# Performance work log

Hardware: AMD Instinct MI355X
Metric: run time of the kernel (lower is better)

Reference implementation:

```python
import jax, jax.numpy as jnp
import numpy as np

N_SAMPLES = 200            # points sampled per ray (n_points in source)
T_HASH = 1 << 19           # hash table size per level (log2_hashmap_size=19)
_PRIMES = jnp.array([1, 2654435761, 805459861], dtype=jnp.uint32)
_CORNERS = jnp.array([[i, j, k] for i in (0, 1) for j in (0, 1) for k in (0, 1)], dtype=jnp.int32)  # [8,3]


def sample_points_along_ray(start, end):
    # start/end: [B,2] in [0,1]. Lerp xy along the ray, z = normalized depth t.
    t = jnp.linspace(0.0, 1.0, N_SAMPLES, dtype=start.dtype)           # [S]
    xy = start[:, None, :] * (1.0 - t)[None, :, None] + end[:, None, :] * t[None, :, None]  # [B,S,2]
    z = jnp.broadcast_to(t[None, :, None], (start.shape[0], N_SAMPLES, 1))
    return jnp.concatenate([xy, z], axis=-1)                            # [B,S,3]


def grid_encode(pts, tables, base_res):
    # pts: [N,3] in [0,1]; tables: [L, T_HASH, D]. Multi-res hash grid + trilinear interp.
    L = tables.shape[0]
    outs = []
    for l in range(L):
        res = base_res * (2 ** l)
        xf = pts * res
        x0 = jnp.floor(xf).astype(jnp.int32)
        w = xf - x0                                                     # [N,3] trilinear weights
        c = x0[:, None, :] + _CORNERS[None]                             # [N,8,3]
        h = c.astype(jnp.uint32) * _PRIMES[None, None, :]
        idx = (h[..., 0] ^ h[..., 1] ^ h[..., 2]) & jnp.uint32(T_HASH - 1)  # [N,8]
        cw = jnp.prod(jnp.where(_CORNERS[None].astype(bool), w[:, None, :], 1.0 - w[:, None, :]), axis=-1)  # [N,8]
        feat = tables[l][idx.astype(jnp.int32)]                         # [N,8,D] gather
        outs.append(jnp.sum(feat * cw[..., None], axis=1))              # [N,D]
    return jnp.concatenate(outs, axis=-1)


def setup_inputs() -> dict:
    key = jax.random.key(0)
    ks = jax.random.split(key, 13)
    B = 16384
    return {
        "x": jax.random.uniform(ks[0], (B, 4), dtype=jnp.float32),
        "table_label": jax.random.normal(ks[1], (5, T_HASH, 1), dtype=jnp.float32),
        "table_rgb": jax.random.normal(ks[2], (6, T_HASH, 4), dtype=jnp.float32),
        "w_label": jax.random.normal(ks[3], (5, 1), dtype=jnp.float32),
        "b_label": jax.random.normal(ks[4], (1,), dtype=jnp.float32),
        "W1": jax.random.normal(ks[5], (120, 64), dtype=jnp.float32) * 0.1,
        "b1": jax.random.normal(ks[6], (64,), dtype=jnp.float32) * 0.1,
        "W2": jax.random.normal(ks[7], (64, 64), dtype=jnp.float32) * 0.1,
        "b2": jax.random.normal(ks[8], (64,), dtype=jnp.float32) * 0.1,
        "W3": jax.random.normal(ks[9], (64, 64), dtype=jnp.float32) * 0.1,
        "b3": jax.random.normal(ks[10], (64,), dtype=jnp.float32) * 0.1,
        "W4": jax.random.normal(ks[11], (64, 3), dtype=jnp.float32) * 0.1,
        "b4": jax.random.normal(ks[12], (3,), dtype=jnp.float32) * 0.1,
    }


def reference(x, table_label, table_rgb, w_label, b_label, W1, b1, W2, b2, W3, b3, W4, b4):
    B = x.shape[0]
    pts = sample_points_along_ray(x[:, :2], x[:, 2:4]).reshape(-1, 3)   # [B*S,3]
    enc_l = grid_encode(pts, table_label, 8).reshape(B, N_SAMPLES, -1)  # [B,S,5]
    label = jax.nn.sigmoid(enc_l @ w_label + b_label)                   # [B,S,1]
    hits = jnp.max(label, axis=1)                                       # [B,1]
    first = jnp.argmax((label > 0.5).astype(jnp.float32), axis=1).reshape(-1)  # [B]
    enc_r = grid_encode(pts, table_rgb, 4).reshape(B, N_SAMPLES, -1)    # [B,S,24]
    rows = jnp.arange(B)
    maxi = N_SAMPLES - 1

    def gather(off):
        return enc_r[rows, jnp.clip(first + off, 0, maxi)]              # [B,24]

    feat = jnp.concatenate([gather(-2), gather(-1), gather(0), gather(1), gather(2)], axis=-1)  # [B,120]
    h = jax.nn.relu(feat @ W1 + b1)
    h = jax.nn.relu(h @ W2 + b2)
    h = jax.nn.relu(h @ W3 + b3)
    rgb = h @ W4 + b4                                                   # [B,3]
    return hits, label, rgb
```

## Files before the change

### kernel.cpp

```cpp
#include <hip/hip_runtime.h>
#include <math.h>
#include <stdint.h>

#define NS 200
#define THASH (1 << 19)
#define TMASK ((1u << 19) - 1u)

__device__ __forceinline__ float sigmoidf_(float v) {
    return 1.0f / (1.0f + __expf(-v));
}

__global__ __launch_bounds__(256) void k_label(
        const float* __restrict__ x,
        const float* __restrict__ tlab,
        const float* __restrict__ wlab, const float* __restrict__ blab,
        float* __restrict__ hits, float* __restrict__ labels,
        int* __restrict__ firsts)
{
    const uint32_t P2 = 2654435761u, P3 = 805459861u;
    const int b = blockIdx.x;
    const int tid = threadIdx.x;
    const int lane = tid & 63;
    const int wid = tid >> 6;
    const float4 ray = *(const float4*)(x + 4 * (size_t)b);

    const int s_eff = tid < NS ? tid : NS - 1;
    const float t = (float)s_eff * (1.0f / 199.0f);
    const float px = ray.x * (1.0f - t) + ray.z * t;
    const float py = ray.y * (1.0f - t) + ray.w * t;
    const float pz = t;

    float acc = blab[0];
    #pragma unroll
    for (int l = 0; l < 5; ++l) {
        const float res = (float)(8 << l);
        const float xf = px * res, yf = py * res, zf = pz * res;
        const float fx = floorf(xf), fy = floorf(yf), fz = floorf(zf);
        const float wx = xf - fx, wy = yf - fy, wz = zf - fz;
        const uint32_t x0 = (uint32_t)(int)fx;
        const uint32_t y0 = (uint32_t)(int)fy;
        const uint32_t z0 = (uint32_t)(int)fz;

        const uint32_t cell = x0 | (y0 << 10) | (z0 << 20);
        const uint32_t prevc = __shfl_up(cell, 1);
        const bool leader = (lane == 0) || (prevc != cell);
        const uint64_t bal = __ballot(leader);
        const uint64_t below = bal & (~0ull >> (63 - lane));
        const int ldr = 63 - __clzll(below);

        float v0 = 0.f, v1 = 0.f, v2 = 0.f, v3 = 0.f,
              v4 = 0.f, v5 = 0.f, v6 = 0.f, v7 = 0.f;
        if (leader) {
            const uint32_t hx0 = x0,      hx1 = x0 + 1u;
            const uint32_t hy0 = y0 * P2, hy1 = hy0 + P2;
            const uint32_t hz0 = z0 * P3, hz1 = hz0 + P3;
            const float* __restrict__ tl = tlab + (size_t)l * THASH;
            v0 = tl[(hx0 ^ hy0 ^ hz0) & TMASK];
            v1 = tl[(hx0 ^ hy0 ^ hz1) & TMASK];
            v2 = tl[(hx0 ^ hy1 ^ hz0) & TMASK];
            v3 = tl[(hx0 ^ hy1 ^ hz1) & TMASK];
            v4 = tl[(hx1 ^ hy0 ^ hz0) & TMASK];
            v5 = tl[(hx1 ^ hy0 ^ hz1) & TMASK];
            v6 = tl[(hx1 ^ hy1 ^ hz0) & TMASK];
            v7 = tl[(hx1 ^ hy1 ^ hz1) & TMASK];
        }
        v0 = __shfl(v0, ldr); v1 = __shfl(v1, ldr);
        v2 = __shfl(v2, ldr); v3 = __shfl(v3, ldr);
        v4 = __shfl(v4, ldr); v5 = __shfl(v5, ldr);
        v6 = __shfl(v6, ldr); v7 = __shfl(v7, ldr);

        const float c00 = fmaf(wz, v1 - v0, v0);
        const float c01 = fmaf(wz, v3 - v2, v2);
        const float c10 = fmaf(wz, v5 - v4, v4);
        const float c11 = fmaf(wz, v7 - v6, v6);
        const float c0 = fmaf(wy, c01 - c00, c00);
        const float c1 = fmaf(wy, c11 - c10, c10);
        const float cv = fmaf(wx, c1 - c0, c0);
        acc = fmaf(cv, wlab[l], acc);
    }

    float lab = -1.0f;
    int cand = NS;
    if (tid < NS) {
        lab = sigmoidf_(acc);
        labels[(size_t)b * NS + tid] = lab;
        if (lab > 0.5f) cand = tid;
    }

    __shared__ float wmax[4];
    __shared__ int wmin[4];
    float m = lab;
    int c = cand;
    #pragma unroll
    for (int off = 32; off > 0; off >>= 1) {
        m = fmaxf(m, __shfl_xor(m, off));
        c = min(c, __shfl_xor(c, off));
    }
    if (lane == 0) { wmax[wid] = m; wmin[wid] = c; }
    __syncthreads();
    if (tid == 0) {
        float mm = fmaxf(fmaxf(wmax[0], wmax[1]), fmaxf(wmax[2], wmax[3]));
        int cc = min(min(wmin[0], wmin[1]), min(wmin[2], wmin[3]));
        hits[b] = mm;
        firsts[b] = (cc >= NS) ? 0 : cc;
    }
}

__global__ __launch_bounds__(256) void k_rgb(
        const float* __restrict__ x,
        const float* __restrict__ trgb,
        const int* __restrict__ firsts,
        const float* __restrict__ W1, const float* __restrict__ b1,
        const float* __restrict__ W2, const float* __restrict__ b2,
        const float* __restrict__ W3, const float* __restrict__ b3,
        const float* __restrict__ W4, const float* __restrict__ b4,
        float* __restrict__ rgb)
{
    const uint32_t P2 = 2654435761u, P3 = 805459861u;
    const int wid = threadIdx.x >> 6;
    const int lane = threadIdx.x & 63;
    const int b = blockIdx.x * 4 + wid;

    __shared__ float feat[4][120];
    __shared__ float hs[4][64];

    const float4 ray = *(const float4*)(x + 4 * (size_t)b);
    const int first = firsts[b];

    const int corner = lane & 7;
    const int group = lane >> 3;
    const int bi = (corner >> 2) & 1, bj = (corner >> 1) & 1, bk = corner & 1;

    #pragma unroll
    for (int it = 0; it < 4; ++it) {
        const int pair = it * 8 + group;
        float vx = 0.f, vy = 0.f, vz = 0.f, vw = 0.f;
        if (pair < 30) {
            const int si = pair / 6;
            const int l = pair % 6;
            int sc = first + si - 2;
            sc = sc < 0 ? 0 : (sc > NS - 1 ? NS - 1 : sc);
            const float t = (float)sc * (1.0f / 199.0f);
            const float px = ray.x * (1.0f - t) + ray.z * t;
            const float py = ray.y * (1.0f - t) + ray.w * t;
            const float pz = t;
            const int res = 4 << l;
            const float xf = px * (float)res, yf = py * (float)res, zf = pz * (float)res;
            const float fx = floorf(xf), fy = floorf(yf), fz = floorf(zf);
            const float wx = xf - fx, wy = yf - fy, wz = zf - fz;
            const uint32_t x0 = (uint32_t)(int)fx, y0 = (uint32_t)(int)fy, z0 = (uint32_t)(int)fz;
            const uint32_t hx = x0 + (uint32_t)bi;
            const uint32_t hy = (y0 + (uint32_t)bj) * P2;
            const uint32_t hz = (z0 + (uint32_t)bk) * P3;
            const uint32_t idx = (hx ^ hy ^ hz) & TMASK;
            const float cw = (bi ? wx : 1.0f - wx) * (bj ? wy : 1.0f - wy) * (bk ? wz : 1.0f - wz);
            const float4 tv = *(const float4*)(trgb + (((size_t)l << 19) + idx) * 4);
            vx = tv.x * cw; vy = tv.y * cw; vz = tv.z * cw; vw = tv.w * cw;
        }
        #pragma unroll
        for (int m = 1; m < 8; m <<= 1) {
            vx += __shfl_xor(vx, m);
            vy += __shfl_xor(vy, m);
            vz += __shfl_xor(vz, m);
            vw += __shfl_xor(vw, m);
        }
        if (corner == 0 && pair < 30) {
            const int si = pair / 6, l = pair % 6;
            float* f = &feat[wid][si * 24 + l * 4];
            f[0] = vx; f[1] = vy; f[2] = vz; f[3] = vw;
        }
    }
    __syncthreads();

    const float* fw = feat[wid];
    float a0 = b1[lane], a1 = 0.f, a2 = 0.f, a3 = 0.f;
    #pragma unroll
    for (int i = 0; i < 120; i += 4) {
        const float4 fv = *(const float4*)(fw + i);
        a0 = fmaf(fv.x, W1[(i + 0) * 64 + lane], a0);
        a1 = fmaf(fv.y, W1[(i + 1) * 64 + lane], a1);
        a2 = fmaf(fv.z, W1[(i + 2) * 64 + lane], a2);
        a3 = fmaf(fv.w, W1[(i + 3) * 64 + lane], a3);
    }
    float h = fmaxf((a0 + a1) + (a2 + a3), 0.0f);

    hs[wid][lane] = h;
    __syncthreads();
    a0 = b2[lane]; a1 = 0.f; a2 = 0.f; a3 = 0.f;
    #pragma unroll
    for (int i = 0; i < 64; i += 4) {
        const float4 hv = *(const float4*)(&hs[wid][i]);
        a0 = fmaf(hv.x, W2[(i + 0) * 64 + lane], a0);
        a1 = fmaf(hv.y, W2[(i + 1) * 64 + lane], a1);
        a2 = fmaf(hv.z, W2[(i + 2) * 64 + lane], a2);
        a3 = fmaf(hv.w, W2[(i + 3) * 64 + lane], a3);
    }
    h = fmaxf((a0 + a1) + (a2 + a3), 0.0f);

    __syncthreads();
    hs[wid][lane] = h;
    __syncthreads();
    a0 = b3[lane]; a1 = 0.f; a2 = 0.f; a3 = 0.f;
    #pragma unroll
    for (int i = 0; i < 64; i += 4) {
        const float4 hv = *(const float4*)(&hs[wid][i]);
        a0 = fmaf(hv.x, W3[(i + 0) * 64 + lane], a0);
        a1 = fmaf(hv.y, W3[(i + 1) * 64 + lane], a1);
        a2 = fmaf(hv.z, W3[(i + 2) * 64 + lane], a2);
        a3 = fmaf(hv.w, W3[(i + 3) * 64 + lane], a3);
    }
    h = fmaxf((a0 + a1) + (a2 + a3), 0.0f);

    __syncthreads();
    hs[wid][lane] = h;
    __syncthreads();
    if (lane < 3) {
        float r = b4[lane];
        #pragma unroll 8
        for (int j = 0; j < 64; ++j) r = fmaf(hs[wid][j], W4[j * 3 + lane], r);
        rgb[(size_t)b * 3 + lane] = r;
    }
}

extern "C" void kernel_launch(void* const* d_in, const int* in_sizes, int n_in,
                              void* d_out, int out_size, void* d_ws, size_t ws_size,
                              hipStream_t stream) {
    const float* x    = (const float*)d_in[0];
    const float* tlab = (const float*)d_in[1];
    const float* trgb = (const float*)d_in[2];
    const float* wlab = (const float*)d_in[3];
    const float* blab = (const float*)d_in[4];
    const float* W1   = (const float*)d_in[5];
    const float* b1   = (const float*)d_in[6];
    const float* W2   = (const float*)d_in[7];
    const float* b2   = (const float*)d_in[8];
    const float* W3   = (const float*)d_in[9];
    const float* b3   = (const float*)d_in[10];
    const float* W4   = (const float*)d_in[11];
    const float* b4   = (const float*)d_in[12];

    const int B = in_sizes[0] / 4;

    float* hits   = (float*)d_out;
    float* labels = hits + B;
    float* rgbout = labels + (size_t)B * NS;
    int* firsts   = (int*)d_ws;

    k_label<<<B, 256, 0, stream>>>(x, tlab, wlab, blab, hits, labels, firsts);
    k_rgb<<<B / 4, 256, 0, stream>>>(x, trgb, firsts,
                                     W1, b1, W2, b2, W3, b3, W4, b4, rgbout);
}
```

Baseline: 120.5 us.

## Derive coarse-level cells from finest grid and batch MLP over 16 rays per block

In the label kernel, the finest-level cell coordinates are computed once and the coarser levels' cells are obtained by right-shifting them. Leader detection uses a masked XOR of neighbouring cells, and the hash corners are built from XOR deltas. The finest level skips the ballot/shuffle dedup and loads directly. In the RGB kernel each block now handles 16 rays, with each wave computing 4 rays per MLP layer so that every weight load is reused across 4 rays. The intent is to cut per-level ALU work and weight traffic, at the cost of more shared memory and registers per block.

```diff
diff --git a/kernel.cpp b/kernel.cpp
--- a/kernel.cpp
+++ b/kernel.cpp
@@ -30,53 +30,90 @@
     const float py = ray.y * (1.0f - t) + ray.w * t;
     const float pz = t;
 
+    const float xf4 = px * 128.0f, yf4 = py * 128.0f, zf4 = pz * 128.0f;
+    const float fx4 = floorf(xf4), fy4 = floorf(yf4), fz4 = floorf(zf4);
+    const uint32_t x4 = (uint32_t)(int)fx4;
+    const uint32_t y4 = (uint32_t)(int)fy4;
+    const uint32_t z4 = (uint32_t)(int)fz4;
+    const uint32_t cell4 = x4 | (y4 << 10) | (z4 << 20);
+    const uint32_t prev = __shfl_up(cell4, 1);
+    const uint32_t diff = cell4 ^ prev;
+
     float acc = blab[0];
+
     #pragma unroll
-    for (int l = 0; l < 5; ++l) {
-        const float res = (float)(8 << l);
-        const float xf = px * res, yf = py * res, zf = pz * res;
-        const float fx = floorf(xf), fy = floorf(yf), fz = floorf(zf);
-        const float wx = xf - fx, wy = yf - fy, wz = zf - fz;
-        const uint32_t x0 = (uint32_t)(int)fx;
-        const uint32_t y0 = (uint32_t)(int)fy;
-        const uint32_t z0 = (uint32_t)(int)fz;
-
-        const uint32_t cell = x0 | (y0 << 10) | (z0 << 20);
-        const uint32_t prevc = __shfl_up(cell, 1);
-        const bool leader = (lane == 0) || (prevc != cell);
+    for (int l = 0; l < 4; ++l) {
+        const int k = 4 - l;
+        const uint32_t fm = 0x3FFu & ~((1u << k) - 1u);
+        const uint32_t m_l = fm | (fm << 10) | (fm << 20);
+        const bool leader = (lane == 0) || ((diff & m_l) != 0u);
         const uint64_t bal = __ballot(leader);
         const uint64_t below = bal & (~0ull >> (63 - lane));
         const int ldr = 63 - __clzll(below);
 
+        const uint32_t x0 = x4 >> k, y0 = y4 >> k, z0 = z4 >> k;
+        const float sc = 1.0f / (float)(1 << k);
+        const float wx = fmaf(xf4, sc, -(float)x0);
+        const float wy = fmaf(yf4, sc, -(float)y0);
+        const float wz = fmaf(zf4, sc, -(float)z0);
+
         float v0 = 0.f, v1 = 0.f, v2 = 0.f, v3 = 0.f,
-              v4 = 0.f, v5 = 0.f, v6 = 0.f, v7 = 0.f;
+              v4v = 0.f, v5 = 0.f, v6 = 0.f, v7 = 0.f;
         if (leader) {
-            const uint32_t hx0 = x0,      hx1 = x0 + 1u;
-            const uint32_t hy0 = y0 * P2, hy1 = hy0 + P2;
-            const uint32_t hz0 = z0 * P3, hz1 = hz0 + P3;
+            const uint32_t hy0 = y0 * P2, hz0 = z0 * P3;
+            const uint32_t base = x0 ^ hy0 ^ hz0;
+            const uint32_t dx = x0 ^ (x0 + 1u);
+            const uint32_t dy = hy0 ^ (hy0 + P2);
+            const uint32_t dz = hz0 ^ (hz0 + P3);
             const float* __restrict__ tl = tlab + (size_t)l * THASH;
-            v0 = tl[(hx0 ^ hy0 ^ hz0) & TMASK];
-            v1 = tl[(hx0 ^ hy0 ^ hz1) & TMASK];
-            v2 = tl[(hx0 ^ hy1 ^ hz0) & TMASK];
-            v3 = tl[(hx0 ^ hy1 ^ hz1) & TMASK];
-            v4 = tl[(hx1 ^ hy0 ^ hz0) & TMASK];
-            v5 = tl[(hx1 ^ hy0 ^ hz1) & TMASK];
-            v6 = tl[(hx1 ^ hy1 ^ hz0) & TMASK];
-            v7 = tl[(hx1 ^ hy1 ^ hz1) & TMASK];
-        }
-        v0 = __shfl(v0, ldr); v1 = __shfl(v1, ldr);
-        v2 = __shfl(v2, ldr); v3 = __shfl(v3, ldr);
-        v4 = __shfl(v4, ldr); v5 = __shfl(v5, ldr);
-        v6 = __shfl(v6, ldr); v7 = __shfl(v7, ldr);
+            v0  = tl[ base                 & TMASK];
+            v1  = tl[(base ^ dz)           & TMASK];
+            v2  = tl[(base ^ dy)           & TMASK];
+            v3  = tl[(base ^ dy ^ dz)      & TMASK];
+            v4v = tl[(base ^ dx)           & TMASK];
+            v5  = tl[(base ^ dx ^ dz)      & TMASK];
+            v6  = tl[(base ^ dx ^ dy)      & TMASK];
+            v7  = tl[(base ^ dx ^ dy ^ dz) & TMASK];
+        }
+        v0  = __shfl(v0, ldr);  v1 = __shfl(v1, ldr);
+        v2  = __shfl(v2, ldr);  v3 = __shfl(v3, ldr);
+        v4v = __shfl(v4v, ldr); v5 = __shfl(v5, ldr);
+        v6  = __shfl(v6, ldr);  v7 = __shfl(v7, ldr);
 
         const float c00 = fmaf(wz, v1 - v0, v0);
         const float c01 = fmaf(wz, v3 - v2, v2);
-        const float c10 = fmaf(wz, v5 - v4, v4);
+        const float c10 = fmaf(wz, v5 - v4v, v4v);
         const float c11 = fmaf(wz, v7 - v6, v6);
         const float c0 = fmaf(wy, c01 - c00, c00);
         const float c1 = fmaf(wy, c11 - c10, c10);
         const float cv = fmaf(wx, c1 - c0, c0);
         acc = fmaf(cv, wlab[l], acc);
+    }
+
+    {
+        const float wx = xf4 - fx4, wy = yf4 - fy4, wz = zf4 - fz4;
+        const uint32_t hy0 = y4 * P2, hz0 = z4 * P3;
+        const uint32_t base = x4 ^ hy0 ^ hz0;
+        const uint32_t dx = x4 ^ (x4 + 1u);
+        const uint32_t dy = hy0 ^ (hy0 + P2);
+        const uint32_t dz = hz0 ^ (hz0 + P3);
+        const float* __restrict__ tl = tlab + (size_t)4 * THASH;
+        const float v0  = tl[ base                 & TMASK];
+        const float v1  = tl[(base ^ dz)           & TMASK];
+        const float v2  = tl[(base ^ dy)           & TMASK];
+        const float v3  = tl[(base ^ dy ^ dz)      & TMASK];
+        const float v4v = tl[(base ^ dx)           & TMASK];
+        const float v5  = tl[(base ^ dx ^ dz)      & TMASK];
+        const float v6  = tl[(base ^ dx ^ dy)      & TMASK];
+        const float v7  = tl[(base ^ dx ^ dy ^ dz) & TMASK];
+        const float c00 = fmaf(wz, v1 - v0, v0);
+        const float c01 = fmaf(wz, v3 - v2, v2);
+        const float c10 = fmaf(wz, v5 - v4v, v4v);
+        const float c11 = fmaf(wz, v7 - v6, v6);
+        const float c0 = fmaf(wy, c01 - c00, c00);
+        const float c1 = fmaf(wy, c11 - c10, c10);
+        const float cv = fmaf(wx, c1 - c0, c0);
+        acc = fmaf(cv, wlab[4], acc);
     }
 
     float lab = -1.0f;
@@ -106,6 +143,7 @@
     }
 }
 
+#define RPB 16
 __global__ __launch_bounds__(256) void k_rgb(
         const float* __restrict__ x,
         const float* __restrict__ trgb,
@@ -117,108 +155,137 @@
         float* __restrict__ rgb)
 {
     const uint32_t P2 = 2654435761u, P3 = 805459861u;
-    const int wid = threadIdx.x >> 6;
-    const int lane = threadIdx.x & 63;
-    const int b = blockIdx.x * 4 + wid;
-
-    __shared__ float feat[4][120];
-    __shared__ float hs[4][64];
-
-    const float4 ray = *(const float4*)(x + 4 * (size_t)b);
-    const int first = firsts[b];
-
-    const int corner = lane & 7;
-    const int group = lane >> 3;
+    const int tid = threadIdx.x;
+    const int lane = tid & 63;
+    const int wid = tid >> 6;
+    const int rayBase = blockIdx.x * RPB;
+
+    __shared__ float feat[RPB][120];
+    __shared__ float hs[RPB][64];
+
+    const int corner = tid & 7;
+    const int rp = tid >> 3;
+    const int ray = rp >> 1;
+    const int pairHalf = rp & 1;
     const int bi = (corner >> 2) & 1, bj = (corner >> 1) & 1, bk = corner & 1;
 
+    const float4 rd = *(const float4*)(x + 4 * (size_t)(rayBase + ray));
+    const int first = firsts[rayBase + ray];
+
     #pragma unroll
-    for (int it = 0; it < 4; ++it) {
-        const int pair = it * 8 + group;
-        float vx = 0.f, vy = 0.f, vz = 0.f, vw = 0.f;
-        if (pair < 30) {
-            const int si = pair / 6;
-            const int l = pair % 6;
-            int sc = first + si - 2;
-            sc = sc < 0 ? 0 : (sc > NS - 1 ? NS - 1 : sc);
-            const float t = (float)sc * (1.0f / 199.0f);
-            const float px = ray.x * (1.0f - t) + ray.z * t;
-            const float py = ray.y * (1.0f - t) + ray.w * t;
-            const float pz = t;
-            const int res = 4 << l;
-            const float xf = px * (float)res, yf = py * (float)res, zf = pz * (float)res;
-            const float fx = floorf(xf), fy = floorf(yf), fz = floorf(zf);
-            const float wx = xf - fx, wy = yf - fy, wz = zf - fz;
-            const uint32_t x0 = (uint32_t)(int)fx, y0 = (uint32_t)(int)fy, z0 = (uint32_t)(int)fz;
-            const uint32_t hx = x0 + (uint32_t)bi;
-            const uint32_t hy = (y0 + (uint32_t)bj) * P2;
-            const uint32_t hz = (z0 + (uint32_t)bk) * P3;
-            const uint32_t idx = (hx ^ hy ^ hz) & TMASK;
-            const float cw = (bi ? wx : 1.0f - wx) * (bj ? wy : 1.0f - wy) * (bk ? wz : 1.0f - wz);
-            const float4 tv = *(const float4*)(trgb + (((size_t)l << 19) + idx) * 4);
-            vx = tv.x * cw; vy = tv.y * cw; vz = tv.z * cw; vw = tv.w * cw;
-        }
+    for (int it = 0; it < 15; ++it) {
+        const int pair = pairHalf * 15 + it;
+        const int si = pair / 6;
+        const int l = pair % 6;
+        int scl = first + si - 2;
+        scl = scl < 0 ? 0 : (scl > NS - 1 ? NS - 1 : scl);
+        const float t = (float)scl * (1.0f / 199.0f);
+        const float px = rd.x * (1.0f - t) + rd.z * t;
+        const float py = rd.y * (1.0f - t) + rd.w * t;
+        const float pz = t;
+        const int res = 4 << l;
+        const float xf = px * (float)res, yf = py * (float)res, zf = pz * (float)res;
+        const float fx = floorf(xf), fy = floorf(yf), fz = floorf(zf);
+        const float wx = xf - fx, wy = yf - fy, wz = zf - fz;
+        const uint32_t x0 = (uint32_t)(int)fx, y0 = (uint32_t)(int)fy, z0 = (uint32_t)(int)fz;
+        const uint32_t hx = x0 + (uint32_t)bi;
+        const uint32_t hy = (y0 + (uint32_t)bj) * P2;
+        const uint32_t hz = (z0 + (uint32_t)bk) * P3;
+        const uint32_t idx = (hx ^ hy ^ hz) & TMASK;
+        const float cw = (bi ? wx : 1.0f - wx) * (bj ? wy : 1.0f - wy) * (bk ? wz : 1.0f - wz);
+        const float4 tv = *(const float4*)(trgb + (((size_t)l << 19) + idx) * 4);
+        float vx = tv.x * cw, vy = tv.y * cw, vz = tv.z * cw, vw = tv.w * cw;
         #pragma unroll
-        for (int m = 1; m < 8; m <<= 1) {
-            vx += __shfl_xor(vx, m);
-            vy += __shfl_xor(vy, m);
-            vz += __shfl_xor(vz, m);
-            vw += __shfl_xor(vw, m);
-        }
-        if (corner == 0 && pair < 30) {
-            const int si = pair / 6, l = pair % 6;
-            float* f = &feat[wid][si * 24 + l * 4];
+        for (int mm = 1; mm < 8; mm <<= 1) {
+            vx += __shfl_xor(vx, mm);
+            vy += __shfl_xor(vy, mm);
+            vz += __shfl_xor(vz, mm);
+            vw += __shfl_xor(vw, mm);
+        }
+        if (corner == 0) {
+            float* f = &feat[ray][si * 24 + l * 4];
             f[0] = vx; f[1] = vy; f[2] = vz; f[3] = vw;
         }
     }
     __syncthreads();
 
-    const float* fw = feat[wid];
-    float a0 = b1[lane], a1 = 0.f, a2 = 0.f, a3 = 0.f;
-    #pragma unroll
+    const int r0 = wid * 4;
+
+    float a0 = b1[lane], a1 = a0, a2 = a0, a3 = a0;
+    #pragma unroll 6
     for (int i = 0; i < 120; i += 4) {
-        const float4 fv = *(const float4*)(fw + i);
-        a0 = fmaf(fv.x, W1[(i + 0) * 64 + lane], a0);
-        a1 = fmaf(fv.y, W1[(i + 1) * 64 + lane], a1);
-        a2 = fmaf(fv.z, W1[(i + 2) * 64 + lane], a2);
-        a3 = fmaf(fv.w, W1[(i + 3) * 64 + lane], a3);
-    }
-    float h = fmaxf((a0 + a1) + (a2 + a3), 0.0f);
-
-    hs[wid][lane] = h;
-    __syncthreads();
-    a0 = b2[lane]; a1 = 0.f; a2 = 0.f; a3 = 0.f;
-    #pragma unroll
+        const float4 f0 = *(const float4*)(&feat[r0 + 0][i]);
+        const float4 f1 = *(const float4*)(&feat[r0 + 1][i]);
+        const float4 f2 = *(const float4*)(&feat[r0 + 2][i]);
+        const float4 f3 = *(const float4*)(&feat[r0 + 3][i]);
+        #pragma unroll
+        for (int j = 0; j < 4; ++j) {
+            const float wv = W1[(i + j) * 64 + lane];
+            a0 = fmaf(((const float*)&f0)[j], wv, a0);
+            a1 = fmaf(((const float*)&f1)[j], wv, a1);
+            a2 = fmaf(((const float*)&f2)[j], wv, a2);
+            a3 = fmaf(((const float*)&f3)[j], wv, a3);
+        }
+    }
+    hs[r0 + 0][lane] = fmaxf(a0, 0.f);
+    hs[r0 + 1][lane] = fmaxf(a1, 0.f);
+    hs[r0 + 2][lane] = fmaxf(a2, 0.f);
+    hs[r0 + 3][lane] = fmaxf(a3, 0.f);
+    __syncthreads();
+
+    a0 = b2[lane]; a1 = a0; a2 = a0; a3 = a0;
+    #pragma unroll 4
     for (int i = 0; i < 64; i += 4) {
-        const float4 hv = *(const float4*)(&hs[wid][i]);
-        a0 = fmaf(hv.x, W2[(i + 0) * 64 + lane], a0);
-        a1 = fmaf(hv.y, W2[(i + 1) * 64 + lane], a1);
-        a2 = fmaf(hv.z, W2[(i + 2) * 64 + lane], a2);
-        a3 = fmaf(hv.w, W2[(i + 3) * 64 + lane], a3);
-    }
-    h = fmaxf((a0 + a1) + (a2 + a3), 0.0f);
-
-    __syncthreads();
-    hs[wid][lane] = h;
-    __syncthreads();
-    a0 = b3[lane]; a1 = 0.f; a2 = 0.f; a3 = 0.f;
-    #pragma unroll
+        const float4 f0 = *(const float4*)(&hs[r0 + 0][i]);
+        const float4 f1 = *(const float4*)(&hs[r0 + 1][i]);
+        const float4 f2 = *(const float4*)(&hs[r0 + 2][i]);
+        const float4 f3 = *(const float4*)(&hs[r0 + 3][i]);
+        #pragma unroll
+        for (int j = 0; j < 4; ++j) {
+            const float wv = W2[(i + j) * 64 + lane];
+            a0 = fmaf(((const float*)&f0)[j], wv, a0);
+            a1 = fmaf(((const float*)&f1)[j], wv, a1);
+            a2 = fmaf(((const float*)&f2)[j], wv, a2);
+            a3 = fmaf(((const float*)&f3)[j], wv, a3);
+        }
+    }
+    __syncthreads();
+    hs[r0 + 0][lane] = fmaxf(a0, 0.f);
+    hs[r0 + 1][lane] = fmaxf(a1, 0.f);
+    hs[r0 + 2][lane] = fmaxf(a2, 0.f);
+    hs[r0 + 3][lane] = fmaxf(a3, 0.f);
+    __syncthreads();
+
+    a0 = b3[lane]; a1 = a0; a2 = a0; a3 = a0;
+    #pragma unroll 4
     for (int i = 0; i < 64; i += 4) {
-        const float4 hv = *(const float4*)(&hs[wid][i]);
-        a0 = fmaf(hv.x, W3[(i + 0) * 64 + lane], a0);
-        a1 = fmaf(hv.y, W3[(i + 1) * 64 + lane], a1);
-        a2 = fmaf(hv.z, W3[(i + 2) * 64 + lane], a2);
-        a3 = fmaf(hv.w, W3[(i + 3) * 64 + lane], a3);
-    }
-    h = fmaxf((a0 + a1) + (a2 + a3), 0.0f);
-
-    __syncthreads();
-    hs[wid][lane] = h;
-    __syncthreads();
-    if (lane < 3) {
-        float r = b4[lane];
+        const float4 f0 = *(const float4*)(&hs[r0 + 0][i]);
+        const float4 f1 = *(const float4*)(&hs[r0 + 1][i]);
+        const float4 f2 = *(const float4*)(&hs[r0 + 2][i]);
+        const float4 f3 = *(const float4*)(&hs[r0 + 3][i]);
+        #pragma unroll
+        for (int j = 0; j < 4; ++j) {
+            const float wv = W3[(i + j) * 64 + lane];
+            a0 = fmaf(((const float*)&f0)[j], wv, a0);
+            a1 = fmaf(((const float*)&f1)[j], wv, a1);
+            a2 = fmaf(((const float*)&f2)[j], wv, a2);
+            a3 = fmaf(((const float*)&f3)[j], wv, a3);
+        }
+    }
+    __syncthreads();
+    hs[r0 + 0][lane] = fmaxf(a0, 0.f);
+    hs[r0 + 1][lane] = fmaxf(a1, 0.f);
+    hs[r0 + 2][lane] = fmaxf(a2, 0.f);
+    hs[r0 + 3][lane] = fmaxf(a3, 0.f);
+    __syncthreads();
+
+    if (lane < 12) {
+        const int r = lane / 3, ch = lane % 3;
+        float acc = b4[ch];
         #pragma unroll 8
-        for (int j = 0; j < 64; ++j) r = fmaf(hs[wid][j], W4[j * 3 + lane], r);
-        rgb[(size_t)b * 3 + lane] = r;
+        for (int j = 0; j < 64; ++j)
+            acc = fmaf(hs[r0 + r][j], W4[j * 3 + ch], acc);
+        rgb[(size_t)(rayBase + r0 + r) * 3 + ch] = acc;
     }
 }
 
@@ -247,6 +314,6 @@
     int* firsts   = (int*)d_ws;
 
     k_label<<<B, 256, 0, stream>>>(x, tlab, wlab, blab, hits, labels, firsts);
-    k_rgb<<<B / 4, 256, 0, stream>>>(x, trgb, firsts,
-                                     W1, b1, W2, b2, W3, b3, W4, b4, rgbout);
+    k_rgb<<<B / RPB, 256, 0, stream>>>(x, trgb, firsts,
+                                       W1, b1, W2, b2, W3, b3, W4, b4, rgbout);
 }
```

Result: faster. 106.2 us (-11.9%).
